# Kernel optimization log

Measured on AMD Instinct MI355X. Metric: run time of the kernel, lower is better.

## Reference

```python
import jax, jax.numpy as jnp
import numpy as np

B, S, HID = 2, 2048, 2048
NH, NKV, D = 32, 8, 64
G = NH // NKV
THETA = 150000.0


def rotate_half(x):
    x1, x2 = x[..., : D // 2], x[..., D // 2 :]
    return jnp.concatenate([-x2, x1], axis=-1)


def setup_inputs() -> dict:
    key = jax.random.key(0)
    ks = jax.random.split(key, 10)
    sc = 0.02
    return {
        "hidden_states": jax.random.normal(ks[0], (B, S, HID), jnp.float32),
        "position_ids": jnp.arange(S, dtype=jnp.int64 if jax.config.jax_enable_x64 else jnp.int32),
        "wq": jax.random.normal(ks[1], (HID, NH * D), jnp.float32) * sc,
        "bq": jax.random.normal(ks[2], (NH * D,), jnp.float32) * sc,
        "wk": jax.random.normal(ks[3], (HID, NKV * D), jnp.float32) * sc,
        "bk": jax.random.normal(ks[4], (NKV * D,), jnp.float32) * sc,
        "wv": jax.random.normal(ks[5], (HID, NKV * D), jnp.float32) * sc,
        "bv": jax.random.normal(ks[6], (NKV * D,), jnp.float32) * sc,
        "wo": jax.random.normal(ks[7], (NH * D, HID), jnp.float32) * sc,
        "bo": jax.random.normal(ks[8], (HID,), jnp.float32) * sc,
    }


def reference(hidden_states, position_ids, wq, bq, wk, bk, wv, bv, wo, bo):
    # projections: [B,S,NH,D] / [B,S,NKV,D] -> head-major
    q = (hidden_states @ wq + bq).reshape(B, S, NH, D).transpose(0, 2, 1, 3)   # [B,NH,S,D]
    k = (hidden_states @ wk + bk).reshape(B, S, NKV, D).transpose(0, 2, 1, 3)  # [B,NKV,S,D]
    v = (hidden_states @ wv + bv).reshape(B, S, NKV, D).transpose(0, 2, 1, 3)

    # HF RoPE: inv_freq over even dims, freqs duplicated across the two halves
    inv_freq = 1.0 / (THETA ** (jnp.arange(0, D, 2, dtype=jnp.float32) / D))   # [D/2]
    freqs = position_ids.astype(jnp.float32)[:, None] * inv_freq[None, :]      # [S,D/2]
    emb = jnp.concatenate([freqs, freqs], axis=-1)                             # [S,D]
    cos = jnp.cos(emb)[None, None]  # [1,1,S,D]
    sin = jnp.sin(emb)[None, None]
    q = q * cos + rotate_half(q) * sin
    k = k * cos + rotate_half(k) * sin

    # GQA: group query heads by kv head instead of repeat_interleave on K/V
    qg = q.reshape(B, NKV, G, S, D)
    scores = jnp.einsum("bkgsd,bktd->bkgst", qg, k) / jnp.sqrt(jnp.float32(D))  # [B,NKV,G,S,S]
    attn = jax.nn.softmax(scores, axis=-1)
    out = jnp.einsum("bkgst,bktd->bkgsd", attn, v)                              # [B,NKV,G,S,D]
    out = out.reshape(B, NH, S, D).transpose(0, 2, 1, 3).reshape(B, S, NH * D)  # [B,S,NH*D]
    return out @ wo + bo
```

## Files before the change

### kernel.cpp

```cpp
#include <hip/hip_runtime.h>
#include <hip/hip_bf16.h>
#include <math.h>

#define B_   2
#define S_   2048
#define HID_ 2048
#define NH_  32
#define NKV_ 8
#define D_   64
#define G_   (NH_/NKV_)
#define M_   (B_*S_)

typedef __hip_bfloat16 bf16;
typedef short bf16x8 __attribute__((ext_vector_type(8)));
typedef float f32x4  __attribute__((ext_vector_type(4)));
typedef unsigned short u16x4 __attribute__((ext_vector_type(4)));

__device__ inline unsigned short f2bfu(float f){
    __hip_bfloat16 h = __float2bfloat16(f);
    return __builtin_bit_cast(unsigned short, h);
}

__device__ __forceinline__ float fexp2(float x){
#if __has_builtin(__builtin_amdgcn_exp2f)
    return __builtin_amdgcn_exp2f(x);
#else
    return exp2f(x);
#endif
}

__device__ __forceinline__ void async16(const void* g, void* l) {
    __builtin_amdgcn_global_load_lds(
        (const __attribute__((address_space(1))) unsigned int*)g,
        (__attribute__((address_space(3))) unsigned int*)l, 16, 0, 0);
}

#define SWZ(r, c) ((c) ^ (((r) & 7) << 3))

#define S_BARRIER() asm volatile("s_barrier" ::: "memory")
__device__ __forceinline__ void vmwait4(){ asm volatile("s_waitcnt vmcnt(4)" ::: "memory"); }
__device__ __forceinline__ void vmwait0(){ asm volatile("s_waitcnt vmcnt(0)" ::: "memory"); }

__device__ __forceinline__ void wtrans_body(
    const float* __restrict__ s0, int N0,
    const float* __restrict__ s1, int N1,
    const float* __restrict__ s2, int N2,
    bf16* __restrict__ dst, int K, int bx, int by,
    unsigned short* __restrict__ tbuf)
{
    unsigned short (*t)[65] = (unsigned short (*)[65])tbuf;
    const int ntile = bx * 64, ktile = by * 64;
    const float* src; int nloc, Nseg;
    if (ntile < N0)           { src = s0; nloc = ntile;           Nseg = N0; }
    else if (ntile < N0 + N1) { src = s1; nloc = ntile - N0;      Nseg = N1; }
    else                      { src = s2; nloc = ntile - N0 - N1; Nseg = N2; }
    const int r  = threadIdx.x >> 4;
    const int c4 = (threadIdx.x & 15) * 4;
    #pragma unroll
    for (int p = 0; p < 4; p++) {
        const int k = p * 16 + r;
        const float4 f = *(const float4*)(src + (size_t)(ktile + k) * Nseg + nloc + c4);
        t[k][c4+0] = f2bfu(f.x); t[k][c4+1] = f2bfu(f.y);
        t[k][c4+2] = f2bfu(f.z); t[k][c4+3] = f2bfu(f.w);
    }
    __syncthreads();
    #pragma unroll
    for (int p = 0; p < 4; p++) {
        const int n = p * 16 + r;
        u16x4 u = { t[c4+0][n], t[c4+1][n], t[c4+2][n], t[c4+3][n] };
        *(u16x4*)((unsigned short*)dst + (size_t)(ntile + n) * K + ktile + c4) = u;
    }
}

__global__ __launch_bounds__(256) void prep_k(
    const float* __restrict__ hs, bf16* __restrict__ hs_b,
    const float* __restrict__ wq, const float* __restrict__ wk,
    const float* __restrict__ wv, bf16* __restrict__ wqkvT,
    const int* __restrict__ pos, float* __restrict__ ctab,
    float* __restrict__ stab)
{
    __shared__ unsigned short tbuf[64 * 65];
    const int bid = blockIdx.x;
    if (bid < 4096) {
        const int i = (bid * 256 + threadIdx.x) * 8;
        const float4 a = *(const float4*)(hs + i);
        const float4 b = *(const float4*)(hs + i + 4);
        uint4 u;
        u.x = (unsigned)f2bfu(a.x) | ((unsigned)f2bfu(a.y) << 16);
        u.y = (unsigned)f2bfu(a.z) | ((unsigned)f2bfu(a.w) << 16);
        u.z = (unsigned)f2bfu(b.x) | ((unsigned)f2bfu(b.y) << 16);
        u.w = (unsigned)f2bfu(b.z) | ((unsigned)f2bfu(b.w) << 16);
        *(uint4*)((unsigned short*)hs_b + i) = u;
    } else if (bid < 5632) {
        const int t = bid - 4096;
        wtrans_body(wq, 2048, wk, 512, wv, 512, wqkvT, HID_,
                    t % 48, t / 48, tbuf);
    } else {
        const int idx = (bid - 5632) * 256 + threadIdx.x;
        const int s = idx >> 5, i = idx & 31;
        const int is64 = (pos[1] == 0);
        const int p = is64 ? pos[2 * s] : pos[s];
        const double inv = exp(-(double)i * (log(150000.0) / 32.0));
        const double f = (double)p * inv;
        ctab[idx] = (float)cos(f);
        stab[idx] = (float)sin(f);
    }
}

__device__ __forceinline__ void slab64(
    const bf16* __restrict__ g, int grow0, int k0,
    unsigned short* lds, int wave, int lane)
{
    const int rr = wave * 8 + (lane >> 3);
    const int cc = ((lane & 7) ^ (lane >> 3)) * 8;
    async16(g + (size_t)(grow0 + rr) * 2048 + k0 + cc, lds + wave * 512);
}

template<int MODE, int BM>
__global__ __launch_bounds__(512, 2) void gemm8p_k(
    const bf16* __restrict__ A, const bf16* __restrict__ WT,
    const float* __restrict__ b0, const float* __restrict__ b1,
    const float* __restrict__ b2,
    bf16* __restrict__ Cq, bf16* __restrict__ Ck, bf16* __restrict__ Cv,
    float* __restrict__ Cout,
    const float* __restrict__ ctab, const float* __restrict__ stab)
{
    constexpr int MT = BM / 32;
    constexpr int PM = MT / 4;
    constexpr int LA = BM * 64;
    constexpr int LB = 256 * 64;
    constexpr int NT = 32;
    __shared__ unsigned short sA[2 * LA];
    __shared__ unsigned short sB[2 * LB];

    const int tid  = threadIdx.x;
    const int wave = tid >> 6, lane = tid & 63;
    const int li   = lane & 15, lj = lane >> 4;
    const int wm   = wave >> 2, wn = wave & 3;

    const int nbx = gridDim.x, nby = gridDim.y;
    const int lin = blockIdx.y * nbx + blockIdx.x;
    const int qq  = (nbx * nby) >> 3;
    const int logical = (lin & 7) * qq + (lin >> 3);
    const int m0 = (logical % nby) * BM;
    const int n0 = (logical / nby) * 256;
    const int swz = li & 7;

    f32x4 acc[MT][4];
    #pragma unroll
    for (int i = 0; i < MT; ++i)
        #pragma unroll
        for (int j = 0; j < 4; ++j)
            acc[i][j] = (f32x4){0.f, 0.f, 0.f, 0.f};

    bf16x8 bfr[4][2];

    auto stageA = [&](int t, int r0) {
        unsigned short* l = sA + (t & 1) * LA + r0 * 64;
        const int k0 = (t & (NT - 1)) * 64;
        slab64(A, m0 + r0,      k0, l,           wave, lane);
        slab64(A, m0 + r0 + 64, k0, l + 64 * 64, wave, lane);
    };
    auto stageB = [&](int t, int r0) {
        unsigned short* l = sB + (t & 1) * LB + r0 * 64;
        const int k0 = (t & (NT - 1)) * 64;
        slab64(WT, n0 + r0,      k0, l,           wave, lane);
        slab64(WT, n0 + r0 + 64, k0, l + 64 * 64, wave, lane);
    };
    auto ldB = [&](int tb) {
        const unsigned short* base = sB + tb * LB;
        #pragma unroll
        for (int nt = 0; nt < 4; ++nt)
            #pragma unroll
            for (int ks = 0; ks < 2; ++ks)
                bfr[nt][ks] = *(const bf16x8*)
                    &base[(wn * 64 + nt * 16 + li) * 64 + ((ks * 4 + lj) ^ swz) * 8];
    };
    auto ldA = [&](int tb, int q, bf16x8 (*af)[2]) {
        const unsigned short* base = sA + tb * LA;
        #pragma unroll
        for (int m = 0; m < PM; ++m)
            #pragma unroll
            for (int ks = 0; ks < 2; ++ks)
                af[m][ks] = *(const bf16x8*)
                    &base[(wm * (BM / 2) + (q * PM + m) * 16 + li) * 64
                          + ((ks * 4 + lj) ^ swz) * 8];
    };
    auto mfma_q = [&](int q, bf16x8 (*af)[2]) {
        __builtin_amdgcn_s_setprio(1);
        #pragma unroll
        for (int ks = 0; ks < 2; ++ks)
            #pragma unroll
            for (int m = 0; m < PM; ++m)
                #pragma unroll
                for (int nt = 0; nt < 4; ++nt)
                    acc[q * PM + m][nt] = __builtin_amdgcn_mfma_f32_16x16x32_bf16(
                        af[m][ks], bfr[nt][ks], acc[q * PM + m][nt], 0, 0, 0);
        __builtin_amdgcn_s_setprio(0);
    };

    stageA(0, 0);
    if constexpr (BM == 256) stageA(0, 128);
    stageB(0, 0); stageB(0, 128);
    stageB(1, 0); stageB(1, 128);
    vmwait4();
    S_BARRIER();

    for (int i = 0; i < NT / 2; ++i) {
        const int ta = 2 * i, tb = 2 * i + 1;
        bf16x8 af0[PM][2], af1[PM][2], af2[PM][2], af3[PM][2];
        ldB(0); ldA(0, 0, af0);
        stageA(tb, 0);
        S_BARRIER(); mfma_q(0, af0); S_BARRIER();
        ldA(0, 1, af1);
        if constexpr (BM == 256) stageA(tb, 128);
        S_BARRIER(); mfma_q(1, af1); S_BARRIER();
        ldA(0, 2, af2);
        stageB(ta + 2, 0);
        S_BARRIER(); mfma_q(2, af2); S_BARRIER();
        ldA(0, 3, af3);
        stageB(ta + 2, 128);
        S_BARRIER(); mfma_q(3, af3);
        vmwait4();
        S_BARRIER();
        ldB(1); ldA(1, 0, af0);
        stageA(ta + 2, 0);
        S_BARRIER(); mfma_q(0, af0); S_BARRIER();
        ldA(1, 1, af1);
        if constexpr (BM == 256) stageA(ta + 2, 128);
        S_BARRIER(); mfma_q(1, af1); S_BARRIER();
        ldA(1, 2, af2);
        stageB(tb + 2, 0);
        S_BARRIER(); mfma_q(2, af2); S_BARRIER();
        ldA(1, 3, af3);
        stageB(tb + 2, 128);
        S_BARRIER(); mfma_q(3, af3);
        vmwait4();
        S_BARRIER();
    }
    vmwait0();
    S_BARRIER();

    if (MODE == 1) {
        #pragma unroll
        for (int mt = 0; mt < MT; ++mt)
            #pragma unroll
            for (int nt = 0; nt < 4; ++nt) {
                const int col = n0 + wn * 64 + nt * 16 + li;
                const float bb = b0[col];
                #pragma unroll
                for (int r = 0; r < 4; ++r) {
                    const int row = m0 + wm * (BM / 2) + mt * 16 + lj * 4 + r;
                    Cout[(size_t)row * HID_ + col] = acc[mt][nt][r] + bb;
                }
            }
        return;
    }

    int seg, cb; const float* bias;
    if (n0 < 2048)      { seg = 0; cb = n0;        bias = b0; }
    else if (n0 < 2560) { seg = 1; cb = n0 - 2048; bias = b1; }
    else                { seg = 2; cb = n0 - 2560; bias = b2; }

    float bl[4];
    #pragma unroll
    for (int nt = 0; nt < 4; ++nt) bl[nt] = bias[cb + wn * 64 + nt * 16 + li];

    if (seg == 2) {
        const int b = m0 >> 11;
        #pragma unroll
        for (int nt = 0; nt < 4; ++nt) {
            const int cseg = cb + wn * 64 + nt * 16 + li;
            const int hv = cseg >> 6, d = cseg & 63;
            #pragma unroll
            for (int mt = 0; mt < MT; ++mt) {
                const int sb = (m0 & (S_ - 1)) + wm * (BM / 2) + mt * 16 + lj * 4;
                u16x4 u = { f2bfu(acc[mt][nt][0] + bl[nt]),
                            f2bfu(acc[mt][nt][1] + bl[nt]),
                            f2bfu(acc[mt][nt][2] + bl[nt]),
                            f2bfu(acc[mt][nt][3] + bl[nt]) };
                *(u16x4*)((unsigned short*)Cv +
                    ((size_t)((b * NKV_ + hv) * 64 + d)) * S_ + sb) = u;
            }
        }
        return;
    }

    const float qs = (seg == 0) ? 0.18033688011112042f : 1.0f;
    #pragma unroll
    for (int mt = 0; mt < MT; ++mt) {
        #pragma unroll
        for (int r = 0; r < 4; ++r) {
            const int row = m0 + wm * (BM / 2) + mt * 16 + lj * 4 + r;
            const int s = row & (S_ - 1);
            const float c0  = ctab[s * 32 + li],      sn0 = stab[s * 32 + li];
            const float c1  = ctab[s * 32 + 16 + li], sn1 = stab[s * 32 + 16 + li];
            const float x0 = acc[mt][0][r] + bl[0];
            const float x1 = acc[mt][1][r] + bl[1];
            const float x2 = acc[mt][2][r] + bl[2];
            const float x3 = acc[mt][3][r] + bl[3];
            const float y0 = (x0 * c0 - x2 * sn0) * qs;
            const float y2 = (x2 * c0 + x0 * sn0) * qs;
            const float y1 = (x1 * c1 - x3 * sn1) * qs;
            const float y3 = (x3 * c1 + x1 * sn1) * qs;
            if (seg == 0) {
                bf16* cp = Cq + (size_t)row * HID_ + n0 + wn * 64 + li;
                cp[0]  = __float2bfloat16(y0);
                cp[16] = __float2bfloat16(y1);
                cp[32] = __float2bfloat16(y2);
                cp[48] = __float2bfloat16(y3);
            } else {
                bf16* cp = Ck + (size_t)row * 512 + cb + wn * 64 + li;
                cp[0]  = __float2bfloat16(y0);
                cp[16] = __float2bfloat16(y1);
                cp[32] = __float2bfloat16(y2);
                cp[48] = __float2bfloat16(y3);
            }
        }
    }
}

__global__ __launch_bounds__(256, 2) void attn_k(
    const bf16* __restrict__ qws, const bf16* __restrict__ kws,
    const bf16* __restrict__ vtw, bf16* __restrict__ ows,
    const float* __restrict__ wo, bf16* __restrict__ woT)
{
    __shared__ unsigned short sMem[24576];

    if (blockIdx.y >= 64) {
        const int t = (blockIdx.y - 64) * 8 + blockIdx.x;
        wtrans_body(wo, 2048, wo, 0, wo, 0, woT, HID_, t & 31, t >> 5, sMem);
        return;
    }

    unsigned short* sK  = sMem;
    unsigned short* sVt = sMem + 4096;
    unsigned short* sP  = sMem + 8192;

    const int tid  = threadIdx.x;
    const int wave = tid >> 6, lane = tid & 63;
    const int li   = lane & 15, lj = lane >> 4;
    const int bh   = blockIdx.y;
    const int q0   = blockIdx.x * 256;
    const int b    = bh / NH_, h = bh % NH_;
    const int hk   = h / G_;

    bf16x8 qf[4][2];
    #pragma unroll
    for (int g = 0; g < 4; g++) {
        const bf16* qp = qws + (size_t)(b * S_ + q0 + wave * 64 + g * 16 + li) * HID_
                         + h * D_ + lj * 8;
        qf[g][0] = *(const bf16x8*)(qp);
        qf[g][1] = *(const bf16x8*)(qp + 32);
    }

    f32x4 o[4][4];
    #pragma unroll
    for (int g = 0; g < 4; g++)
        #pragma unroll
        for (int mt = 0; mt < 4; mt++) o[g][mt] = (f32x4){0.f, 0.f, 0.f, 0.f};
    float mr[4] = {-1e30f, -1e30f, -1e30f, -1e30f};
    float ll[4] = {0.f, 0.f, 0.f, 0.f};

    const int srow = tid >> 2, scol = (tid & 3) * 16;
    const bf16* kb = kws + (size_t)b * S_ * 512 + hk * 64;
    const bf16* vb = vtw + (size_t)((b * NKV_ + hk) * 64) * S_;
    unsigned short* sp = sP + wave * (64 * 64);

    uint4 pk0, pk1, pv0, pv1;
    {
        const uint4* kp = (const uint4*)(kb + (size_t)srow * 512 + scol);
        const uint4* vp = (const uint4*)(vb + (size_t)srow * S_ + scol);
        pk0 = kp[0]; pk1 = kp[1]; pv0 = vp[0]; pv1 = vp[1];
    }

    for (int kt = 0; kt < S_; kt += 64) {
        __syncthreads();
        *(uint4*)&sK [srow * 64 + SWZ(srow, scol)]     = pk0;
        *(uint4*)&sK [srow * 64 + SWZ(srow, scol + 8)] = pk1;
        *(uint4*)&sVt[srow * 64 + SWZ(srow, scol)]     = pv0;
        *(uint4*)&sVt[srow * 64 + SWZ(srow, scol + 8)] = pv1;
        __syncthreads();

        if (kt + 64 < S_) {
            const uint4* kp = (const uint4*)(kb + (size_t)(kt + 64 + srow) * 512 + scol);
            const uint4* vp = (const uint4*)(vb + (size_t)srow * S_ + kt + 64 + scol);
            pk0 = kp[0]; pk1 = kp[1]; pv0 = vp[0]; pv1 = vp[1];
        }

        bf16x8 kf[4][2];
        #pragma unroll
        for (int nt = 0; nt < 4; nt++)
            #pragma unroll
            for (int ks = 0; ks < 2; ks++)
                kf[nt][ks] = *(const bf16x8*)&sK[(nt * 16 + li) * 64
                                                 + SWZ(li, ks * 32 + lj * 8)];

        #pragma unroll
        for (int g = 0; g < 4; g++) {
            f32x4 c[4];
            __builtin_amdgcn_s_setprio(1);
            #pragma unroll
            for (int nt = 0; nt < 4; nt++) {
                c[nt] = (f32x4){0.f, 0.f, 0.f, 0.f};
                #pragma unroll
                for (int ks = 0; ks < 2; ks++)
                    c[nt] = __builtin_amdgcn_mfma_f32_16x16x32_bf16(
                        kf[nt][ks], qf[g][ks], c[nt], 0, 0, 0);
            }
            __builtin_amdgcn_s_setprio(0);

            float cm = c[0][0];
            #pragma unroll
            for (int nt = 0; nt < 4; nt++)
                #pragma unroll
                for (int r = 0; r < 4; r++) cm = fmaxf(cm, c[nt][r]);
            cm = fmaxf(cm, __shfl_xor(cm, 16));
            cm = fmaxf(cm, __shfl_xor(cm, 32));
            if (!__all(cm - mr[g] <= 8.0f)) {
                const float mnew = fmaxf(mr[g], cm);
                const float al   = fexp2(mr[g] - mnew);
                mr[g] = mnew;
                ll[g] *= al;
                #pragma unroll
                for (int mt = 0; mt < 4; mt++) o[g][mt] *= al;
            }
            float rs = 0.f;
            #pragma unroll
            for (int nt = 0; nt < 4; nt++) {
                const float e0 = fexp2(c[nt][0] - mr[g]);
                const float e1 = fexp2(c[nt][1] - mr[g]);
                const float e2 = fexp2(c[nt][2] - mr[g]);
                const float e3 = fexp2(c[nt][3] - mr[g]);
                rs += (e0 + e1) + (e2 + e3);
                u16x4 u = { f2bfu(e0), f2bfu(e1), f2bfu(e2), f2bfu(e3) };
                *(u16x4*)&sp[(g * 16 + li) * 64 + SWZ(li, nt * 16 + lj * 4)] = u;
            }
            ll[g] += rs;
        }

        bf16x8 vf[4][2];
        #pragma unroll
        for (int mt = 0; mt < 4; mt++)
            #pragma unroll
            for (int ks = 0; ks < 2; ks++)
                vf[mt][ks] = *(const bf16x8*)&sVt[(mt * 16 + li) * 64
                                                  + SWZ(li, ks * 32 + lj * 8)];

        __builtin_amdgcn_s_setprio(1);
        #pragma unroll
        for (int g = 0; g < 4; g++) {
            #pragma unroll
            for (int ks = 0; ks < 2; ks++) {
                const bf16x8 pf = *(const bf16x8*)&sp[(g * 16 + li) * 64
                                                      + SWZ(li, ks * 32 + lj * 8)];
                #pragma unroll
                for (int mt = 0; mt < 4; mt++)
                    o[g][mt] = __builtin_amdgcn_mfma_f32_16x16x32_bf16(
                        vf[mt][ks], pf, o[g][mt], 0, 0, 0);
            }
        }
        __builtin_amdgcn_s_setprio(0);
    }

    #pragma unroll
    for (int g = 0; g < 4; g++) {
        float l = ll[g];
        l += __shfl_xor(l, 16);
        l += __shfl_xor(l, 32);
        const float inv = 1.0f / l;
        bf16* op = ows + (size_t)(b * S_ + q0 + wave * 64 + g * 16 + li) * HID_ + h * D_;
        #pragma unroll
        for (int mt = 0; mt < 4; mt++) {
            u16x4 u = { f2bfu(o[g][mt][0] * inv), f2bfu(o[g][mt][1] * inv),
                        f2bfu(o[g][mt][2] * inv), f2bfu(o[g][mt][3] * inv) };
            *(u16x4*)((unsigned short*)op + mt * 16 + lj * 4) = u;
        }
    }
}

extern "C" void kernel_launch(void* const* d_in, const int* in_sizes, int n_in,
                              void* d_out, int out_size, void* d_ws, size_t ws_size,
                              hipStream_t stream)
{
    const float* hs  = (const float*)d_in[0];
    const int*   pos = (const int*)d_in[1];
    const float* wq = (const float*)d_in[2];
    const float* bq = (const float*)d_in[3];
    const float* wk = (const float*)d_in[4];
    const float* bk = (const float*)d_in[5];
    const float* wv = (const float*)d_in[6];
    const float* bv = (const float*)d_in[7];
    const float* wo = (const float*)d_in[8];
    const float* bo = (const float*)d_in[9];

    char* ws = (char*)d_ws;
    float* ctab  = (float*)(ws);
    float* stab  = (float*)(ws + (256u << 10));
    bf16*  k_ws  = (bf16*)(ws + (512u << 10));
    bf16*  v_t   = (bf16*)(ws + (512u << 10) + (4u  << 20));
    bf16*  q_ws  = (bf16*)(ws + (512u << 10) + (8u  << 20));
    bf16*  hs_b  = (bf16*)(ws + (512u << 10) + (24u << 20));
    bf16*  o_ws  = hs_b;
    bf16*  wqkvT = (bf16*)(ws + (512u << 10) + (40u << 20));
    bf16*  woT   = wqkvT;

    prep_k<<<dim3(5888), dim3(256), 0, stream>>>(
        hs, hs_b, wq, wk, wv, wqkvT, pos, ctab, stab);

    gemm8p_k<0, 256><<<dim3(12, 16), dim3(512), 0, stream>>>(
        hs_b, wqkvT, bq, bk, bv, q_ws, k_ws, v_t, nullptr, ctab, stab);

    attn_k<<<dim3(8, 192), dim3(256), 0, stream>>>(
        q_ws, k_ws, v_t, o_ws, wo, woT);

    gemm8p_k<1, 128><<<dim3(8, 32), dim3(512), 0, stream>>>(
        o_ws, woT, bo, nullptr, nullptr, nullptr, nullptr, nullptr,
        (float*)d_out, nullptr, nullptr);
}
```

Before: 321.0 us.

## Halve GEMM pipeline phases and batch all QK MFMAs before softmax in attention

The GEMM main loop now works in two halves per K-tile instead of four quarter phases. Each half issues the whole A or B tile stage at once, which cuts the number of barriers per tile roughly in half. In the attention kernel, all 16 QK^T score tiles for the four query groups are computed up front, and the V fragments are loaded from LDS before the softmax loop. This gives the MFMA unit longer independent runs and hides LDS latency. The trade-off is higher register pressure from holding 16 accumulators and larger A fragment arrays, plus coarser overlap of global loads with compute.

```diff
diff --git a/kernel.cpp b/kernel.cpp
--- a/kernel.cpp
+++ b/kernel.cpp
@@ -117,7 +117,7 @@
 }
 
 template<int MODE, int BM>
-__global__ __launch_bounds__(512, 2) void gemm8p_k(
+__global__ __launch_bounds__(512, 2) void gemm4p_k(
     const bf16* __restrict__ A, const bf16* __restrict__ WT,
     const float* __restrict__ b0, const float* __restrict__ b1,
     const float* __restrict__ b2,
@@ -126,7 +126,7 @@
     const float* __restrict__ ctab, const float* __restrict__ stab)
 {
     constexpr int MT = BM / 32;
-    constexpr int PM = MT / 4;
+    constexpr int PM = MT / 2;
     constexpr int LA = BM * 64;
     constexpr int LB = 256 * 64;
     constexpr int NT = 32;
@@ -155,20 +155,22 @@
 
     bf16x8 bfr[4][2];
 
-    auto stageA = [&](int t, int r0) {
-        unsigned short* l = sA + (t & 1) * LA + r0 * 64;
+    auto stageAf = [&](int t) {
+        unsigned short* l = sA + (t & 1) * LA;
         const int k0 = (t & (NT - 1)) * 64;
-        slab64(A, m0 + r0,      k0, l,           wave, lane);
-        slab64(A, m0 + r0 + 64, k0, l + 64 * 64, wave, lane);
+        #pragma unroll
+        for (int i = 0; i < BM / 64; ++i)
+            slab64(A, m0 + i * 64, k0, l + i * 64 * 64, wave, lane);
     };
-    auto stageB = [&](int t, int r0) {
-        unsigned short* l = sB + (t & 1) * LB + r0 * 64;
+    auto stageBf = [&](int t) {
+        unsigned short* l = sB + (t & 1) * LB;
         const int k0 = (t & (NT - 1)) * 64;
-        slab64(WT, n0 + r0,      k0, l,           wave, lane);
-        slab64(WT, n0 + r0 + 64, k0, l + 64 * 64, wave, lane);
+        #pragma unroll
+        for (int j = 0; j < 4; ++j)
+            slab64(WT, n0 + j * 64, k0, l + j * 64 * 64, wave, lane);
     };
-    auto ldB = [&](int tb) {
-        const unsigned short* base = sB + tb * LB;
+    auto ldB = [&](int tb_) {
+        const unsigned short* base = sB + tb_ * LB;
         #pragma unroll
         for (int nt = 0; nt < 4; ++nt)
             #pragma unroll
@@ -176,17 +178,17 @@
                 bfr[nt][ks] = *(const bf16x8*)
                     &base[(wn * 64 + nt * 16 + li) * 64 + ((ks * 4 + lj) ^ swz) * 8];
     };
-    auto ldA = [&](int tb, int q, bf16x8 (*af)[2]) {
-        const unsigned short* base = sA + tb * LA;
+    auto ldA = [&](int tb_, int h, bf16x8 (*af)[2]) {
+        const unsigned short* base = sA + tb_ * LA;
         #pragma unroll
         for (int m = 0; m < PM; ++m)
             #pragma unroll
             for (int ks = 0; ks < 2; ++ks)
                 af[m][ks] = *(const bf16x8*)
-                    &base[(wm * (BM / 2) + (q * PM + m) * 16 + li) * 64
+                    &base[(wm * (BM / 2) + (h * PM + m) * 16 + li) * 64
                           + ((ks * 4 + lj) ^ swz) * 8];
     };
-    auto mfma_q = [&](int q, bf16x8 (*af)[2]) {
+    auto mfma_h = [&](int h, bf16x8 (*af)[2]) {
         __builtin_amdgcn_s_setprio(1);
         #pragma unroll
         for (int ks = 0; ks < 2; ++ks)
@@ -194,47 +196,32 @@
             for (int m = 0; m < PM; ++m)
                 #pragma unroll
                 for (int nt = 0; nt < 4; ++nt)
-                    acc[q * PM + m][nt] = __builtin_amdgcn_mfma_f32_16x16x32_bf16(
-                        af[m][ks], bfr[nt][ks], acc[q * PM + m][nt], 0, 0, 0);
+                    acc[h * PM + m][nt] = __builtin_amdgcn_mfma_f32_16x16x32_bf16(
+                        af[m][ks], bfr[nt][ks], acc[h * PM + m][nt], 0, 0, 0);
         __builtin_amdgcn_s_setprio(0);
     };
 
-    stageA(0, 0);
-    if constexpr (BM == 256) stageA(0, 128);
-    stageB(0, 0); stageB(0, 128);
-    stageB(1, 0); stageB(1, 128);
+    stageAf(0); stageBf(0); stageBf(1);
     vmwait4();
     S_BARRIER();
 
     for (int i = 0; i < NT / 2; ++i) {
         const int ta = 2 * i, tb = 2 * i + 1;
-        bf16x8 af0[PM][2], af1[PM][2], af2[PM][2], af3[PM][2];
-        ldB(0); ldA(0, 0, af0);
-        stageA(tb, 0);
-        S_BARRIER(); mfma_q(0, af0); S_BARRIER();
-        ldA(0, 1, af1);
-        if constexpr (BM == 256) stageA(tb, 128);
-        S_BARRIER(); mfma_q(1, af1); S_BARRIER();
-        ldA(0, 2, af2);
-        stageB(ta + 2, 0);
-        S_BARRIER(); mfma_q(2, af2); S_BARRIER();
-        ldA(0, 3, af3);
-        stageB(ta + 2, 128);
-        S_BARRIER(); mfma_q(3, af3);
+        bf16x8 afh[PM][2];
+        ldB(0); ldA(0, 0, afh);
+        stageAf(tb);
+        S_BARRIER(); mfma_h(0, afh); S_BARRIER();
+        ldA(0, 1, afh);
+        stageBf(ta + 2);
+        S_BARRIER(); mfma_h(1, afh);
         vmwait4();
         S_BARRIER();
-        ldB(1); ldA(1, 0, af0);
-        stageA(ta + 2, 0);
-        S_BARRIER(); mfma_q(0, af0); S_BARRIER();
-        ldA(1, 1, af1);
-        if constexpr (BM == 256) stageA(ta + 2, 128);
-        S_BARRIER(); mfma_q(1, af1); S_BARRIER();
-        ldA(1, 2, af2);
-        stageB(tb + 2, 0);
-        S_BARRIER(); mfma_q(2, af2); S_BARRIER();
-        ldA(1, 3, af3);
-        stageB(tb + 2, 128);
-        S_BARRIER(); mfma_q(3, af3);
+        ldB(1); ldA(1, 0, afh);
+        stageAf(ta + 2);
+        S_BARRIER(); mfma_h(0, afh); S_BARRIER();
+        ldA(1, 1, afh);
+        stageBf(tb + 2);
+        S_BARRIER(); mfma_h(1, afh);
         vmwait4();
         S_BARRIER();
     }
@@ -396,25 +383,38 @@
                 kf[nt][ks] = *(const bf16x8*)&sK[(nt * 16 + li) * 64
                                                  + SWZ(li, ks * 32 + lj * 8)];
 
+        f32x4 c[4][4];
+        __builtin_amdgcn_s_setprio(1);
+        #pragma unroll
+        for (int g = 0; g < 4; g++)
+            #pragma unroll
+            for (int nt = 0; nt < 4; nt++) {
+                f32x4 t = (f32x4){0.f, 0.f, 0.f, 0.f};
+                t = __builtin_amdgcn_mfma_f32_16x16x32_bf16(kf[nt][0], qf[g][0], t, 0, 0, 0);
+                t = __builtin_amdgcn_mfma_f32_16x16x32_bf16(kf[nt][1], qf[g][1], t, 0, 0, 0);
+                c[g][nt] = t;
+            }
+        __builtin_amdgcn_s_setprio(0);
+
+        bf16x8 vf[4][2];
+        #pragma unroll
+        for (int mt = 0; mt < 4; mt++)
+            #pragma unroll
+            for (int ks = 0; ks < 2; ks++)
+                vf[mt][ks] = *(const bf16x8*)&sVt[(mt * 16 + li) * 64
+                                                  + SWZ(li, ks * 32 + lj * 8)];
+
         #pragma unroll
         for (int g = 0; g < 4; g++) {
-            f32x4 c[4];
-            __builtin_amdgcn_s_setprio(1);
-            #pragma unroll
-            for (int nt = 0; nt < 4; nt++) {
-                c[nt] = (f32x4){0.f, 0.f, 0.f, 0.f};
-                #pragma unroll
-                for (int ks = 0; ks < 2; ks++)
-                    c[nt] = __builtin_amdgcn_mfma_f32_16x16x32_bf16(
-                        kf[nt][ks], qf[g][ks], c[nt], 0, 0, 0);
-            }
-            __builtin_amdgcn_s_setprio(0);
-
-            float cm = c[0][0];
-            #pragma unroll
-            for (int nt = 0; nt < 4; nt++)
-                #pragma unroll
-                for (int r = 0; r < 4; r++) cm = fmaxf(cm, c[nt][r]);
+            float m0a = fmaxf(fmaxf(c[g][0][0], c[g][0][1]),
+                              fmaxf(c[g][0][2], c[g][0][3]));
+            float m1a = fmaxf(fmaxf(c[g][1][0], c[g][1][1]),
+                              fmaxf(c[g][1][2], c[g][1][3]));
+            float m2a = fmaxf(fmaxf(c[g][2][0], c[g][2][1]),
+                              fmaxf(c[g][2][2], c[g][2][3]));
+            float m3a = fmaxf(fmaxf(c[g][3][0], c[g][3][1]),
+                              fmaxf(c[g][3][2], c[g][3][3]));
+            float cm = fmaxf(fmaxf(m0a, m1a), fmaxf(m2a, m3a));
             cm = fmaxf(cm, __shfl_xor(cm, 16));
             cm = fmaxf(cm, __shfl_xor(cm, 32));
             if (!__all(cm - mr[g] <= 8.0f)) {
@@ -428,24 +428,16 @@
             float rs = 0.f;
             #pragma unroll
             for (int nt = 0; nt < 4; nt++) {
-                const float e0 = fexp2(c[nt][0] - mr[g]);
-                const float e1 = fexp2(c[nt][1] - mr[g]);
-                const float e2 = fexp2(c[nt][2] - mr[g]);
-                const float e3 = fexp2(c[nt][3] - mr[g]);
+                const float e0 = fexp2(c[g][nt][0] - mr[g]);
+                const float e1 = fexp2(c[g][nt][1] - mr[g]);
+                const float e2 = fexp2(c[g][nt][2] - mr[g]);
+                const float e3 = fexp2(c[g][nt][3] - mr[g]);
                 rs += (e0 + e1) + (e2 + e3);
                 u16x4 u = { f2bfu(e0), f2bfu(e1), f2bfu(e2), f2bfu(e3) };
                 *(u16x4*)&sp[(g * 16 + li) * 64 + SWZ(li, nt * 16 + lj * 4)] = u;
             }
             ll[g] += rs;
         }
-
-        bf16x8 vf[4][2];
-        #pragma unroll
-        for (int mt = 0; mt < 4; mt++)
-            #pragma unroll
-            for (int ks = 0; ks < 2; ks++)
-                vf[mt][ks] = *(const bf16x8*)&sVt[(mt * 16 + li) * 64
-                                                  + SWZ(li, ks * 32 + lj * 8)];
 
         __builtin_amdgcn_s_setprio(1);
         #pragma unroll
@@ -508,13 +500,13 @@
     prep_k<<<dim3(5888), dim3(256), 0, stream>>>(
         hs, hs_b, wq, wk, wv, wqkvT, pos, ctab, stab);
 
-    gemm8p_k<0, 256><<<dim3(12, 16), dim3(512), 0, stream>>>(
+    gemm4p_k<0, 256><<<dim3(12, 16), dim3(512), 0, stream>>>(
         hs_b, wqkvT, bq, bk, bv, q_ws, k_ws, v_t, nullptr, ctab, stab);
 
     attn_k<<<dim3(8, 192), dim3(256), 0, stream>>>(
         q_ws, k_ws, v_t, o_ws, wo, woT);
 
-    gemm8p_k<1, 128><<<dim3(8, 32), dim3(512), 0, stream>>>(
+    gemm4p_k<1, 128><<<dim3(8, 32), dim3(512), 0, stream>>>(
         o_ws, woT, bo, nullptr, nullptr, nullptr, nullptr, nullptr,
         (float*)d_out, nullptr, nullptr);
 }
```

Result: no change. 324.3 us (+1.0%).
